# Kernel tuning notes

Hardware: AMD Instinct MI355X
Metric: run time of the kernel (lower is better)

## Reference

```python
import jax, jax.numpy as jnp
import numpy as np

B, S, T, V, E, H, D, A = 16, 128, 128, 32000, 512, 512, 512, 512
ENC = 2 * H  # bidirectional encoder output dim
NEG = -1e9


def _w(key, shape, scale=0.05):
    return scale * jax.random.normal(key, shape, dtype=jnp.float32)


def setup_inputs() -> dict:
    key = jax.random.key(0)
    ks = jax.random.split(key, 26)
    src = jax.random.randint(ks[0], (B, S), 1, V)
    tgt = jax.random.randint(ks[1], (B, T), 1, V)
    src_lens = jnp.full((B,), S, dtype=jnp.int32)  # full-length sequences (pack == identity)
    return dict(
        src=src, src_lens=src_lens, tgt=tgt,
        enc_embed=_w(ks[2], (V, E)).at[0].set(0.0),   # padding_idx=0
        Wih_f=_w(ks[3], (4 * H, E)), Whh_f=_w(ks[4], (4 * H, H)),
        bih_f=_w(ks[5], (4 * H,)), bhh_f=_w(ks[6], (4 * H,)),
        Wih_b=_w(ks[7], (4 * H, E)), Whh_b=_w(ks[8], (4 * H, H)),
        bih_b=_w(ks[9], (4 * H,)), bhh_b=_w(ks[10], (4 * H,)),
        Wbh=_w(ks[11], (D, 2 * H)), bbh=_w(ks[12], (D,)),
        Wbc=_w(ks[13], (D, 2 * H)), bbc=_w(ks[14], (D,)),
        Wh_att=_w(ks[15], (A, ENC)), Ws_att=_w(ks[16], (A, D)), v_att=_w(ks[17], (A,)),
        dec_embed=_w(ks[18], (V, E)).at[0].set(0.0),  # padding_idx=0
        Wih_d=_w(ks[19], (4 * D, E + ENC)), Whh_d=_w(ks[20], (4 * D, D)),
        bih_d=_w(ks[21], (4 * D,)), bhh_d=_w(ks[22], (4 * D,)),
        Wfc=_w(ks[23], (V, D + ENC)), bfc=_w(ks[24], (V,)),
    )


def _lstm_cell(x, h, c, Wih, Whh, bih, bhh):
    # PyTorch gate order: i, f, g, o
    g = x @ Wih.T + h @ Whh.T + (bih + bhh)
    i, f, gg, o = jnp.split(g, 4, axis=-1)
    c = jax.nn.sigmoid(f) * c + jax.nn.sigmoid(i) * jnp.tanh(gg)
    h = jax.nn.sigmoid(o) * jnp.tanh(c)
    return h, c


def _run_lstm(xs, Wih, Whh, bih, bhh, hdim):
    # xs: [S, B, E] -> (hs [S, B, hdim], h_last, c_last)
    b = xs.shape[1]
    h0 = jnp.zeros((b, hdim), xs.dtype)

    def step(carry, x):
        h, c = carry
        h, c = _lstm_cell(x, h, c, Wih, Whh, bih, bhh)
        return (h, c), h

    (hT, cT), hs = jax.lax.scan(step, (h0, h0), xs)
    return hs, hT, cT


def reference(src, src_lens, tgt, enc_embed, Wih_f, Whh_f, bih_f, bhh_f,
              Wih_b, Whh_b, bih_b, bhh_b, Wbh, bbh, Wbc, bbc,
              Wh_att, Ws_att, v_att, dec_embed, Wih_d, Whh_d, bih_d, bhh_d,
              Wfc, bfc):
    # ---- BiLSTM encoder (src_lens == S, so packing is the identity) ----
    emb = enc_embed[src]                      # [B, S, E]
    xs = jnp.swapaxes(emb, 0, 1)              # [S, B, E]
    hs_f, hf, _ = _run_lstm(xs, Wih_f, Whh_f, bih_f, bhh_f, H)
    hs_b, hb, _ = _run_lstm(xs[::-1], Wih_b, Whh_b, bih_b, bhh_b, H)
    hs_b = hs_b[::-1]
    enc_out = jnp.swapaxes(jnp.concatenate([hs_f, hs_b], axis=-1), 0, 1)  # [B, S, 2H]

    # ---- bridge (num_layers = 1) ----
    h_cat = jnp.concatenate([hf, hb], axis=-1)  # [B, 2H]
    h0 = jnp.tanh(h_cat @ Wbh.T + bbh)          # [B, D]
    c_cat = jnp.concatenate([hf, hb], axis=-1)
    c0 = jnp.tanh(c_cat @ Wbc.T + bbc)

    mask = jnp.arange(S)[None, :] < src_lens[:, None]  # [B, S]
    enc_proj = jnp.einsum('bse,ae->bsa', enc_out, Wh_att)  # W_h(enc_out), hoisted

    # ---- decoder loop, teacher_forcing = 1.0 ----
    def dec_step(carry, inp_t):
        h, c = carry
        # Bahdanau attention on top-layer hidden state
        score = jnp.einsum('bsa,a->bs', jnp.tanh(enc_proj + (h @ Ws_att.T)[:, None, :]), v_att)
        score = jnp.where(mask, score, NEG)
        attn = jax.nn.softmax(score, axis=-1)
        ctx = jnp.einsum('bs,bse->be', attn, enc_out)       # [B, 2H]
        x = jnp.concatenate([dec_embed[inp_t], ctx], axis=-1)  # [B, E+2H]
        h, c = _lstm_cell(x, h, c, Wih_d, Whh_d, bih_d, bhh_d)
        logits = jnp.concatenate([h, ctx], axis=-1) @ Wfc.T + bfc  # [B, V]
        return (h, c), logits

    inps = tgt[:, :-1].T  # [T-1, B]
    _, logits = jax.lax.scan(dec_step, (h0, c0), inps)
    return jnp.swapaxes(logits, 0, 1)  # [B, T-1, V]
```

## Files before the change

kernel.cpp:

```cpp
#include <hip/hip_runtime.h>

typedef __bf16 bf16x8 __attribute__((ext_vector_type(8)));
typedef float f32x4 __attribute__((ext_vector_type(4)));
typedef unsigned short us;
typedef unsigned long long ull;

#define DEV static __device__ __forceinline__

DEV float bf2f(us u){ union { unsigned u; float f; } x; x.u = ((unsigned)u) << 16; return x.f; }
DEV us f2bf(float f){
  union { float f; unsigned u; } x; x.f = f;
  unsigned r = x.u + 0x7fffu + ((x.u >> 16) & 1u);
  return (us)(r >> 16);
}
DEV unsigned pack2(us lo, us hi){ return (unsigned)lo | ((unsigned)hi << 16); }
DEV float sigm(float x){ return 1.0f / (1.0f + expf(-x)); }
DEV float tanh_fast(float x){ float e = __expf(2.0f * x); return 1.0f - 2.0f / (e + 1.0f); }
DEV void unpk2(unsigned u, float& a, float& b){ a = bf2f((us)u); b = bf2f((us)(u >> 16)); }

DEV unsigned ld4v(const unsigned* p){ return __hip_atomic_load(p, __ATOMIC_RELAXED, __HIP_MEMORY_SCOPE_AGENT); }
DEV ull ld8v(const void* p){ return __hip_atomic_load((const ull*)p, __ATOMIC_RELAXED, __HIP_MEMORY_SCOPE_AGENT); }
DEV void st4v(unsigned* p, unsigned v){ __hip_atomic_store(p, v, __ATOMIC_RELAXED, __HIP_MEMORY_SCOPE_AGENT); }

DEV void gridbar3(unsigned* arr, unsigned ep){
  __syncthreads();
  if (threadIdx.x == 0)
    __hip_atomic_store(arr + (size_t)blockIdx.x * 16, ep, __ATOMIC_RELEASE, __HIP_MEMORY_SCOPE_AGENT);
  if (threadIdx.x < 128){
    while (__hip_atomic_load(arr + (size_t)threadIdx.x * 16, __ATOMIC_RELAXED, __HIP_MEMORY_SCOPE_AGENT) < ep)
      __builtin_amdgcn_s_sleep(4);
  }
  __syncthreads();
}

DEV void groupbar(unsigned* gbase, int slot, unsigned ep){
  __syncthreads();
  if (threadIdx.x == 0)
    __hip_atomic_store(gbase + slot * 16, ep, __ATOMIC_RELEASE, __HIP_MEMORY_SCOPE_AGENT);
  if (threadIdx.x < 8){
    while (__hip_atomic_load(gbase + threadIdx.x * 16, __ATOMIC_RELAXED, __HIP_MEMORY_SCOPE_AGENT) < ep)
      __builtin_amdgcn_s_sleep(2);
  }
  __syncthreads();
}

__global__ void k_f2bf(const float4* __restrict__ in, uint2* __restrict__ out, long n4){
  long stride = (long)gridDim.x * blockDim.x;
  for (long i = (long)blockIdx.x * blockDim.x + threadIdx.x; i < n4; i += stride){
    float4 v = in[i];
    uint2 o; o.x = pack2(f2bf(v.x), f2bf(v.y)); o.y = pack2(f2bf(v.z), f2bf(v.w));
    out[i] = o;
  }
}

__global__ void k_bias3(const float* a0, const float* b0, float* o0,
                        const float* a1, const float* b1, float* o1,
                        const float* a2, const float* b2, float* o2){
  int i = blockIdx.x * 256 + threadIdx.x;
  o0[i] = a0[i] + b0[i];
  o1[i] = a1[i] + b1[i];
  o2[i] = a2[i] + b2[i];
}

__global__ void k_embed(const int* __restrict__ tok, const float* __restrict__ table,
                        us* __restrict__ out){
  int r = blockIdx.x;
  int b = r & 15, pos = r >> 4;
  int idx = tok[b * 128 + pos];
  float4 v = ((const float4*)(table + (size_t)idx * 512))[threadIdx.x];
  uint2 o; o.x = pack2(f2bf(v.x), f2bf(v.y)); o.y = pack2(f2bf(v.z), f2bf(v.w));
  ((uint2*)(out + (size_t)r * 512))[threadIdx.x] = o;
}

template<int MODE>
__global__ __launch_bounds__(256)
void gemm_bt(const us* __restrict__ A, int lda,
             const us* __restrict__ B, int ldb,
             const float* __restrict__ bias,
             void* __restrict__ Cv, int ldc, int K, int mvalid)
{
  __shared__ __align__(16) us As[128 * 64];
  __shared__ __align__(16) us Bs[128 * 64];
  const int tid  = threadIdx.x;
  const int lane = tid & 63, wid = tid >> 6;
  const int wm = (wid >> 1) * 64, wn = (wid & 1) * 64;
  const us* Ab = A + (size_t)blockIdx.y * 128 * lda;
  const us* Bb = B + (size_t)blockIdx.x * 128 * ldb;

  f32x4 acc[4][4] = {};
  bf16x8 ga[4], gb[4];

  #pragma unroll
  for (int r = 0; r < 4; r++){
    int c = tid + r * 256;
    ga[r] = *(const bf16x8*)(Ab + (size_t)(c >> 3) * lda + (c & 7) * 8);
    gb[r] = *(const bf16x8*)(Bb + (size_t)(c >> 3) * ldb + (c & 7) * 8);
  }
  const int nt = K >> 6;
  for (int t = 0; t < nt; t++){
    #pragma unroll
    for (int r = 0; r < 4; r++){
      int c = tid + r * 256;
      int slot = ((c >> 3) * 8 + ((c & 7) ^ ((c >> 3) & 7))) * 8;
      *(bf16x8*)(As + slot) = ga[r];
      *(bf16x8*)(Bs + slot) = gb[r];
    }
    __syncthreads();
    if (t + 1 < nt){
      int k0 = (t + 1) * 64;
      #pragma unroll
      for (int r = 0; r < 4; r++){
        int c = tid + r * 256;
        ga[r] = *(const bf16x8*)(Ab + (size_t)(c >> 3) * lda + k0 + (c & 7) * 8);
        gb[r] = *(const bf16x8*)(Bb + (size_t)(c >> 3) * ldb + k0 + (c & 7) * 8);
      }
    }
    #pragma unroll
    for (int kk = 0; kk < 2; kk++){
      bf16x8 av[4], bv[4];
      #pragma unroll
      for (int i = 0; i < 4; i++){
        int ra = wm + i * 16 + (lane & 15);
        int ua = (kk * 4 + (lane >> 4)) ^ (ra & 7);
        av[i] = *(const bf16x8*)(As + (ra * 8 + ua) * 8);
        int rb = wn + i * 16 + (lane & 15);
        int ub = (kk * 4 + (lane >> 4)) ^ (rb & 7);
        bv[i] = *(const bf16x8*)(Bs + (rb * 8 + ub) * 8);
      }
      #pragma unroll
      for (int i = 0; i < 4; i++)
        #pragma unroll
        for (int j = 0; j < 4; j++)
          acc[i][j] = __builtin_amdgcn_mfma_f32_16x16x32_bf16(av[i], bv[j], acc[i][j], 0, 0, 0);
    }
    if (t + 1 < nt) __syncthreads();
  }

  const int cb = lane & 15, rb4 = (lane >> 4) * 4;
  #pragma unroll
  for (int i = 0; i < 4; i++){
    #pragma unroll
    for (int j = 0; j < 4; j++){
      #pragma unroll
      for (int r = 0; r < 4; r++){
        int row = blockIdx.y * 128 + wm + i * 16 + rb4 + r;
        int col = blockIdx.x * 128 + wn + j * 16 + cb;
        float v = acc[i][j][r];
        if (bias) v += bias[col];
        if (MODE == 0) ((float*)Cv)[(size_t)row * ldc + col] = v;
        else           ((us*)Cv)[(size_t)row * ldc + col] = f2bf(v);
      }
    }
  }
}

__global__ __launch_bounds__(256)
void enc_persist4(const float* __restrict__ gin_f, const float* __restrict__ gin_b,
                  const us* __restrict__ whhf_bf, const us* __restrict__ whhb_bf,
                  us* __restrict__ enc_out_bf,
                  unsigned* __restrict__ arr)
{
  __shared__ __align__(16) us Wt[2][1024][8];
  __shared__ __align__(16) us Hrow[2][16][520];
  __shared__ __align__(16) f32x4 P[2][4][64];
  __shared__ float gl[2][16][17];
  __shared__ float hvout[2][16][4];

  const int bx = blockIdx.x, tid = threadIdx.x;
  const int lane = tid & 63, wv = tid >> 6;

  for (int d = 0; d < 2; d++){
    const us* srcw = d ? whhb_bf : whhf_bf;
    for (int u = tid; u < 1024; u += 256){
      int ks = u >> 6, ch = (u >> 4) & 3, v = u & 15;
      int n = (v & 3) * 512 + bx * 4 + (v >> 2);
      *(bf16x8*)Wt[d][u] = *(const bf16x8*)(srcw + (size_t)n * 512 + ks * 32 + ch * 8);
    }
  }

  float creg = 0.0f;
  const int cd = (tid >> 6) & 1, cb = tid & 15, cj = (tid >> 4) & 3;

  for (int t = 0; t < 128; t++){
    if (t == 0){
      #pragma unroll
      for (int r = 0; r < 8; r++){
        int u = tid + r * 256;
        int d = u >> 10, b = (u >> 6) & 15, s16 = u & 63;
        *(ull*)&Hrow[d][b][s16 * 8]     = 0ull;
        *(ull*)&Hrow[d][b][s16 * 8 + 4] = 0ull;
      }
    } else {
      #pragma unroll
      for (int r = 0; r < 8; r++){
        int u = tid + r * 256;
        int d = u >> 10, b = (u >> 6) & 15, s16 = u & 63;
        int sp = d ? (128 - t) : (t - 1);
        const us* s = enc_out_bf + ((size_t)b * 128 + sp) * 1024 + d * 512 + s16 * 8;
        ull lo = ld8v(s), hi = ld8v(s + 4);
        *(ull*)&Hrow[d][b][s16 * 8]     = lo;
        *(ull*)&Hrow[d][b][s16 * 8 + 4] = hi;
      }
    }
    __syncthreads();
    #pragma unroll
    for (int d = 0; d < 2; d++){
      f32x4 acc = {};
      #pragma unroll
      for (int m = 0; m < 4; m++){
        int ks = wv * 4 + m;
        int ch = lane >> 4, b = lane & 15;
        acc = __builtin_amdgcn_mfma_f32_16x16x32_bf16(*(const bf16x8*)&Hrow[d][b][ks * 32 + ch * 8],
                                                      *(const bf16x8*)Wt[d][(ks * 4 + ch) * 16 + b],
                                                      acc, 0, 0, 0);
      }
      P[d][wv][lane] = acc;
    }
    __syncthreads();
    if (wv < 2){
      int d = wv;
      f32x4 sum = (P[d][0][lane] + P[d][1][lane]) + (P[d][2][lane] + P[d][3][lane]);
      int v = lane & 15;
      int n = (v & 3) * 512 + bx * 4 + (v >> 2);
      int s_in = d ? (127 - t) : t;
      const float* gg = (d ? gin_b : gin_f) + (size_t)s_in * 16 * 2048 + n;
      #pragma unroll
      for (int r = 0; r < 4; r++){
        int b = (lane >> 4) * 4 + r;
        gl[d][v][b] = sum[r] + gg[(size_t)b * 2048];
      }
    }
    __syncthreads();
    if (tid < 128){
      float ig = sigm (gl[cd][cj * 4 + 0][cb]);
      float fg = sigm (gl[cd][cj * 4 + 1][cb]);
      float g2 = tanhf(gl[cd][cj * 4 + 2][cb]);
      float og = sigm (gl[cd][cj * 4 + 3][cb]);
      float cn = fg * creg + ig * g2;
      float hv = og * tanhf(cn);
      creg = cn;
      hvout[cd][cb][cj] = hv;
    }
    __syncthreads();
    if (tid < 64){
      int d = tid >> 5, rem = tid & 31, b = rem & 15, jp = rem >> 4;
      int s_in = d ? (127 - t) : t;
      st4v((unsigned*)(enc_out_bf + ((size_t)b * 128 + s_in) * 1024 + d * 512 + bx * 4 + jp * 2),
           pack2(f2bf(hvout[d][b][jp * 2]), f2bf(hvout[d][b][jp * 2 + 1])));
    }
    if (t != 127) gridbar3(arr, t + 1);
  }
}

__global__ __launch_bounds__(512)
void k_h0c0(const us* __restrict__ enc_out_bf, const float* __restrict__ Wbh, const float* __restrict__ bbh,
            const float* __restrict__ Wbc, const float* __restrict__ bbc,
            us* __restrict__ h0_bf, float* __restrict__ c_dec)
{
  __shared__ float hc[1024];
  int b = blockIdx.x >> 1, which = blockIdx.x & 1;
  int tid = threadIdx.x;
  hc[tid]       = bf2f(enc_out_bf[((size_t)b * 128 + 127) * 1024 + tid]);
  hc[512 + tid] = bf2f(enc_out_bf[((size_t)b * 128 + 0)   * 1024 + 512 + tid]);
  __syncthreads();
  const float* W = which ? Wbc : Wbh;
  float acc = (which ? bbc : bbh)[tid];
  const float* wr = W + (size_t)tid * 1024;
  for (int k = 0; k < 1024; k += 4){
    float4 w = *(const float4*)(wr + k);
    acc += w.x * hc[k] + w.y * hc[k + 1] + w.z * hc[k + 2] + w.w * hc[k + 3];
  }
  float v = tanhf(acc);
  if (which) c_dec[b * 512 + tid] = v;
  else       h0_bf[b * 512 + tid] = f2bf(v);
}

#define SMEM_BYTES 162464

__global__ __launch_bounds__(256)
void dec_fused3(const us* __restrict__ h0_bf, const float* __restrict__ c_dec0,
                const float* __restrict__ Ws_att, const float* __restrict__ v_att,
                const us* __restrict__ enc_proj_bf, const us* __restrict__ enc_out_bf,
                const int* __restrict__ src_lens, const float* __restrict__ gin_d,
                const us* __restrict__ whhd_bf, const us* __restrict__ wihd_bf,
                float* __restrict__ pscore_g,
                us* __restrict__ hctx,
                const us* __restrict__ wfc, const float* __restrict__ bfc,
                float* __restrict__ out,
                unsigned* __restrict__ arr, unsigned* __restrict__ arrG,
                unsigned* __restrict__ tdone)
{
  __shared__ __align__(16) char smem[SMEM_BYTES];
  const int tid = threadIdx.x;

  if (blockIdx.x >= 128){
    us* As = (us*)smem;
    us* Bs = (us*)(smem + 32768);
    const int lane = tid & 63, wid = tid >> 6;
    const int wm = wid * 64;
    for (int tile = blockIdx.x - 128; tile < 2000; tile += 128){
      int rt = tile / 250, ct = tile - rt * 250;
      unsigned need = (rt == 7) ? 127u : (unsigned)(16 * rt + 16);
      if (tid == 0){
        while (ld4v(tdone) < need) __builtin_amdgcn_s_sleep(8);
      }
      __syncthreads();
      const us* Ab = hctx + (size_t)rt * 256 * 1536;
      const us* Bb = wfc  + (size_t)ct * 128 * 1536;
      f32x4 acc[4][8] = {};
      bf16x8 ga[8], gb[4];
      #pragma unroll
      for (int r = 0; r < 8; r++){
        int cc = tid + r * 256;
        int row = cc >> 3, piece = cc & 7;
        bool val = (rt * 256 + row) < 2032;
        union { ull q[2]; bf16x8 v; } u;
        const us* p = Ab + (size_t)row * 1536 + piece * 8;
        u.q[0] = val ? ld8v(p) : 0ull;
        u.q[1] = val ? ld8v(p + 4) : 0ull;
        ga[r] = u.v;
      }
      #pragma unroll
      for (int r = 0; r < 4; r++){
        int cc = tid + r * 256;
        gb[r] = __builtin_nontemporal_load((const bf16x8*)(Bb + (size_t)(cc >> 3) * 1536 + (cc & 7) * 8));
      }
      for (int tk = 0; tk < 24; tk++){
        #pragma unroll
        for (int r = 0; r < 8; r++){
          int cc = tid + r * 256;
          int slot = ((cc >> 3) * 8 + ((cc & 7) ^ ((cc >> 3) & 7))) * 8;
          *(bf16x8*)(As + slot) = ga[r];
        }
        #pragma unroll
        for (int r = 0; r < 4; r++){
          int cc = tid + r * 256;
          int slot = ((cc >> 3) * 8 + ((cc & 7) ^ ((cc >> 3) & 7))) * 8;
          *(bf16x8*)(Bs + slot) = gb[r];
        }
        __syncthreads();
        if (tk + 1 < 24){
          int k0 = (tk + 1) * 64;
          #pragma unroll
          for (int r = 0; r < 8; r++){
            int cc = tid + r * 256;
            int row = cc >> 3, piece = cc & 7;
            bool val = (rt * 256 + row) < 2032;
            union { ull q[2]; bf16x8 v; } u;
            const us* p = Ab + (size_t)row * 1536 + k0 + piece * 8;
            u.q[0] = val ? ld8v(p) : 0ull;
            u.q[1] = val ? ld8v(p + 4) : 0ull;
            ga[r] = u.v;
          }
          #pragma unroll
          for (int r = 0; r < 4; r++){
            int cc = tid + r * 256;
            gb[r] = __builtin_nontemporal_load((const bf16x8*)(Bb + (size_t)(cc >> 3) * 1536 + k0 + (cc & 7) * 8));
          }
        }
        #pragma unroll
        for (int kk = 0; kk < 2; kk++){
          bf16x8 av[4], bv[8];
          #pragma unroll
          for (int i = 0; i < 4; i++){
            int ra = wm + i * 16 + (lane & 15);
            int ua = (kk * 4 + (lane >> 4)) ^ (ra & 7);
            av[i] = *(const bf16x8*)(As + (ra * 8 + ua) * 8);
          }
          #pragma unroll
          for (int j = 0; j < 8; j++){
            int rb = j * 16 + (lane & 15);
            int ub = (kk * 4 + (lane >> 4)) ^ (rb & 7);
            bv[j] = *(const bf16x8*)(Bs + (rb * 8 + ub) * 8);
          }
          #pragma unroll
          for (int i = 0; i < 4; i++)
            #pragma unroll
            for (int j = 0; j < 8; j++)
              acc[i][j] = __builtin_amdgcn_mfma_f32_16x16x32_bf16(av[i], bv[j], acc[i][j], 0, 0, 0);
        }
        if (tk + 1 < 24) __syncthreads();
      }
      const int cbl = lane & 15, rb4 = (lane >> 4) * 4;
      #pragma unroll
      for (int i = 0; i < 4; i++){
        #pragma unroll
        for (int j = 0; j < 8; j++){
          #pragma unroll
          for (int r = 0; r < 4; r++){
            int row = rt * 256 + wm + i * 16 + rb4 + r;
            int col = ct * 128 + j * 16 + cbl;
            if (row < 2032){
              float v = acc[i][j][r] + bfc[col];
              int tt = row >> 4, b = row & 15;
              out[((size_t)b * 127 + tt) * 32000 + col] = v;
            }
          }
        }
      }
    }
    return;
  }

  us (*Wh)[8]      = (us(*)[8])(smem);
  us (*Wc)[8]      = (us(*)[8])(smem + 16384);
  us (*Ws64)[520]  = (us(*)[520])(smem + 49152);
  us (*Xrow)[1032] = (us(*)[1032])(smem + 115712);
  f32x4 (*P)[64]   = (f32x4(*)[64])(smem + 148736);
  float (*g1l)[17] = (float(*)[17])(smem + 152832);
  float (*gl)[17]  = (float(*)[17])(smem + 153920);
  float* vl64      = (float*)(smem + 155008);
  float (*hsp)[64] = (float(*)[64])(smem + 155264);
  float* hs_own    = (float*)(smem + 156288);
  float (*pall)[128] = (float(*)[128])(smem + 156544);
  float* att       = (float*)(smem + 160640);
  float (*cred)[128] = (float(*)[128])(smem + 161152);
  float* sred      = (float*)(smem + 162176);
  float (*hvs)[4]  = (float(*)[4])(smem + 162208);

  const int bx = blockIdx.x;
  const int lane = tid & 63, wv = tid >> 6;
  const int bB = bx & 15, sQ = bx >> 4;
  unsigned* gbase = arrG + bB * 128;

  for (int u = tid; u < 1024; u += 256){
    int ks = u >> 6, ch = (u >> 4) & 3, v = u & 15;
    int n = (v & 3) * 512 + bx * 4 + (v >> 2);
    *(bf16x8*)Wh[u] = *(const bf16x8*)(whhd_bf + (size_t)n * 512 + ks * 32 + ch * 8);
  }
  for (int u = tid; u < 2048; u += 256){
    int ks = u >> 6, ch = (u >> 4) & 3, v = u & 15;
    int n = (v & 3) * 512 + bx * 4 + (v >> 2);
    *(bf16x8*)Wc[u] = *(const bf16x8*)(wihd_bf + (size_t)n * 1536 + 512 + ks * 32 + ch * 8);
  }
  for (int u = tid; u < 32768; u += 256){
    int a = u >> 9, k = u & 511;
    Ws64[a][k] = f2bf(Ws_att[(size_t)(sQ * 64 + a) * 512 + k]);
  }
  if (tid < 64) vl64[tid] = v_att[sQ * 64 + tid];
  const int slen = src_lens[bB];

  float creg = 0.0f;
  if (tid < 64) creg = c_dec0[(tid & 15) * 512 + bx * 4 + (tid >> 4)];

  for (int t = 0; t < 127; t++){
    const us* hsrc = t ? (hctx + (size_t)(t - 1) * 16 * 1536) : h0_bf;
    const int hstride = t ? 1536 : 512;

    #pragma unroll
    for (int r = 0; r < 4; r++){
      int u = tid + r * 256;
      int b = u >> 6, s16 = u & 63;
      const us* s = hsrc + (size_t)b * hstride + s16 * 8;
      ull lo = ld8v(s), hi = ld8v(s + 4);
      *(ull*)&Xrow[b][s16 * 8]     = lo;
      *(ull*)&Xrow[b][s16 * 8 + 4] = hi;
    }
    __syncthreads();
    {
      f32x4 acc = {};
      #pragma unroll
      for (int m = 0; m < 4; m++){
        int ks = wv * 4 + m;
        int ch = lane >> 4, b = lane & 15;
        acc = __builtin_amdgcn_mfma_f32_16x16x32_bf16(*(const bf16x8*)&Xrow[b][ks * 32 + ch * 8],
                                                      *(const bf16x8*)Wh[(ks * 4 + ch) * 16 + b],
                                                      acc, 0, 0, 0);
      }
      P[wv][lane] = acc;
    }
    {
      const us* wr = Ws64[lane] + wv * 128;
      const us* xr = Xrow[bB] + wv * 128;
      float s = 0.f;
      #pragma unroll
      for (int k = 0; k < 128; k += 8){
        bf16x8 xv = *(const bf16x8*)(xr + k);
        bf16x8 wv8 = *(const bf16x8*)(wr + k);
        #pragma unroll
        for (int e = 0; e < 8; e++) s += (float)xv[e] * (float)wv8[e];
      }
      hsp[wv][lane] = s;
    }
    __syncthreads();
    if (wv == 0){
      f32x4 sum = (P[0][lane] + P[1][lane]) + (P[2][lane] + P[3][lane]);
      int v = lane & 15;
      int n = (v & 3) * 512 + bx * 4 + (v >> 2);
      #pragma unroll
      for (int r = 0; r < 4; r++){
        int b = (lane >> 4) * 4 + r;
        g1l[v][b] = sum[r] + gin_d[((size_t)t * 16 + b) * 2048 + n];
      }
    }
    if (tid < 64) hs_own[tid] = hsp[0][tid] + hsp[1][tid] + hsp[2][tid] + hsp[3][tid];
    __syncthreads();
    {
      int s = tid >> 1, half = tid & 1;
      const us* er = enc_proj_bf + ((size_t)bB * 128 + s) * 512 + sQ * 64 + half * 32;
      const float* hb = hs_own + half * 32;
      const float* vp = vl64 + half * 32;
      float sv = 0.f;
      #pragma unroll
      for (int a = 0; a < 32; a += 8){
        uint4 u4 = *(const uint4*)(er + a);
        float e0,e1,e2,e3,e4,e5,e6,e7;
        unpk2(u4.x,e0,e1); unpk2(u4.y,e2,e3); unpk2(u4.z,e4,e5); unpk2(u4.w,e6,e7);
        sv += vp[a+0]*tanh_fast(e0+hb[a+0]) + vp[a+1]*tanh_fast(e1+hb[a+1])
            + vp[a+2]*tanh_fast(e2+hb[a+2]) + vp[a+3]*tanh_fast(e3+hb[a+3])
            + vp[a+4]*tanh_fast(e4+hb[a+4]) + vp[a+5]*tanh_fast(e5+hb[a+5])
            + vp[a+6]*tanh_fast(e6+hb[a+6]) + vp[a+7]*tanh_fast(e7+hb[a+7]);
      }
      sv += __shfl_xor(sv, 1);
      if (half == 0)
        st4v((unsigned*)&pscore_g[(size_t)bB * 1024 + sQ * 128 + s], __float_as_uint(sv));
    }

    groupbar(gbase, sQ, t + 1);

    for (int u = tid; u < 1024; u += 256)
      (&pall[0][0])[u] = __uint_as_float(ld4v((unsigned*)&pscore_g[(size_t)bB * 1024 + u]));
    __syncthreads();
    {
      float e = 0.f;
      if (tid < 128){
        float sc = ((pall[0][tid] + pall[1][tid]) + (pall[2][tid] + pall[3][tid]))
                 + ((pall[4][tid] + pall[5][tid]) + (pall[6][tid] + pall[7][tid]));
        e = (tid < slen) ? __expf(sc) : 0.f;
        att[tid] = e;
      }
      float ss = e;
      #pragma unroll
      for (int o = 32; o; o >>= 1) ss += __shfl_xor(ss, o);
      if (lane == 0) sred[wv] = ss;
    }
    __syncthreads();
    {
      int kk = tid & 127, half = tid >> 7;
      const float* ab = att + half * 64;
      const us* er = enc_out_bf + ((size_t)(bB * 128 + half * 64)) * 1024 + sQ * 128 + kk;
      float s = 0.f;
      #pragma unroll 8
      for (int s2 = 0; s2 < 64; s2++)
        s += ab[s2] * bf2f(er[(size_t)s2 * 1024]);
      cred[half][kk] = s;
    }
    __syncthreads();
    if (tid < 64){
      float inv = 1.0f / (sred[0] + sred[1] + sred[2] + sred[3]);
      int kk2 = tid * 2;
      float c0 = (cred[0][kk2]     + cred[1][kk2])     * inv;
      float c1 = (cred[0][kk2 + 1] + cred[1][kk2 + 1]) * inv;
      st4v((unsigned*)(hctx + ((size_t)t * 16 + bB) * 1536 + 512 + sQ * 128 + kk2),
           pack2(f2bf(c0), f2bf(c1)));
    }

    gridbar3(arr, 2 * t + 1);

    #pragma unroll
    for (int r = 0; r < 8; r++){
      int u = tid + r * 256;
      int b = u >> 7, s16 = u & 127;
      const us* s = hctx + ((size_t)t * 16 + b) * 1536 + 512 + s16 * 8;
      ull lo = ld8v(s), hi = ld8v(s + 4);
      *(ull*)&Xrow[b][s16 * 8]     = lo;
      *(ull*)&Xrow[b][s16 * 8 + 4] = hi;
    }
    __syncthreads();
    {
      f32x4 acc = {};
      #pragma unroll
      for (int m = 0; m < 8; m++){
        int ks = wv * 8 + m;
        int ch = lane >> 4, b = lane & 15;
        acc = __builtin_amdgcn_mfma_f32_16x16x32_bf16(*(const bf16x8*)&Xrow[b][ks * 32 + ch * 8],
                                                      *(const bf16x8*)Wc[(ks * 4 + ch) * 16 + b],
                                                      acc, 0, 0, 0);
      }
      P[wv][lane] = acc;
    }
    __syncthreads();
    if (wv == 0){
      f32x4 sum = (P[0][lane] + P[1][lane]) + (P[2][lane] + P[3][lane]);
      int v = lane & 15;
      #pragma unroll
      for (int r = 0; r < 4; r++){
        int b = (lane >> 4) * 4 + r;
        gl[v][b] = sum[r] + g1l[v][b];
      }
    }
    __syncthreads();
    if (tid < 64){
      int b2 = tid & 15, joff = tid >> 4;
      float ig = sigm (gl[joff * 4 + 0][b2]);
      float fg = sigm (gl[joff * 4 + 1][b2]);
      float g2 = tanhf(gl[joff * 4 + 2][b2]);
      float og = sigm (gl[joff * 4 + 3][b2]);
      float cn = fg * creg + ig * g2;
      float hv = og * tanhf(cn);
      creg = cn;
      hvs[b2][joff] = hv;
    }
    __syncthreads();
    if (tid < 32){
      int b = tid & 15, jp = tid >> 4;
      st4v((unsigned*)(hctx + ((size_t)t * 16 + b) * 1536 + bx * 4 + jp * 2),
           pack2(f2bf(hvs[b][jp * 2]), f2bf(hvs[b][jp * 2 + 1])));
    }
    gridbar3(arr, 2 * t + 2);
    if (bx == 0 && tid == 0)
      __hip_atomic_store(tdone, (unsigned)(t + 1), __ATOMIC_RELEASE, __HIP_MEMORY_SCOPE_AGENT);
  }
}

extern "C" void kernel_launch(void* const* d_in, const int* in_sizes, int n_in,
                              void* d_out, int out_size, void* d_ws, size_t ws_size,
                              hipStream_t stream)
{
  const int*   src       = (const int*)d_in[0];
  const int*   src_lens  = (const int*)d_in[1];
  const int*   tgt       = (const int*)d_in[2];
  const float* enc_embed = (const float*)d_in[3];
  const float* Wih_f = (const float*)d_in[4];
  const float* Whh_f = (const float*)d_in[5];
  const float* bih_f = (const float*)d_in[6];
  const float* bhh_f = (const float*)d_in[7];
  const float* Wih_b = (const float*)d_in[8];
  const float* Whh_b = (const float*)d_in[9];
  const float* bih_b = (const float*)d_in[10];
  const float* bhh_b = (const float*)d_in[11];
  const float* Wbh = (const float*)d_in[12];
  const float* bbh = (const float*)d_in[13];
  const float* Wbc = (const float*)d_in[14];
  const float* bbc = (const float*)d_in[15];
  const float* Wh_att = (const float*)d_in[16];
  const float* Ws_att = (const float*)d_in[17];
  const float* v_att  = (const float*)d_in[18];
  const float* dec_embed = (const float*)d_in[19];
  const float* Wih_d = (const float*)d_in[20];
  const float* Whh_d = (const float*)d_in[21];
  const float* bih_d = (const float*)d_in[22];
  const float* bhh_d = (const float*)d_in[23];
  const float* Wfc = (const float*)d_in[24];
  const float* bfc = (const float*)d_in[25];
  float* out = (float*)d_out;

  char* base = (char*)d_ws;
  size_t off = 0;
  auto take = [&](size_t bytes) -> char* {
    char* p = base + off;
    off += (bytes + 255) & ~(size_t)255;
    return p;
  };
  us* wfc_bf    = (us*)take((size_t)32000 * 1536 * 2);
  us* emb_e     = (us*)take((size_t)2048 * 512 * 2);
  us* emb_d     = (us*)take((size_t)2048 * 512 * 2);
  us* wihf_bf   = (us*)take((size_t)2048 * 512 * 2);
  us* wihb_bf   = (us*)take((size_t)2048 * 512 * 2);
  us* wihd_bf   = (us*)take((size_t)2048 * 1536 * 2);
  us* whhf_bf   = (us*)take((size_t)2048 * 512 * 2);
  us* whhb_bf   = (us*)take((size_t)2048 * 512 * 2);
  us* whhd_bf   = (us*)take((size_t)2048 * 512 * 2);
  us* whatt_bf  = (us*)take((size_t)512 * 1024 * 2);
  float* gin_f    = (float*)take((size_t)2048 * 2048 * 4);
  float* gin_b    = (float*)take((size_t)2048 * 2048 * 4);
  float* gin_d    = (float*)take((size_t)2048 * 2048 * 4);
  us* enc_out_bf  = (us*)take((size_t)2048 * 1024 * 2);
  us* enc_proj_bf = (us*)take((size_t)2048 * 512 * 2);
  us* hctx        = (us*)take((size_t)2048 * 1536 * 2);
  us* h0_bf       = (us*)take((size_t)16 * 512 * 2);
  float* c_dec    = (float*)take((size_t)16 * 512 * 4);
  float* pscore_g = (float*)take((size_t)16 * 1024 * 4);
  float* bias_f = (float*)take(2048 * 4);
  float* bias_b = (float*)take(2048 * 4);
  float* bias_d = (float*)take(2048 * 4);
  unsigned* arrE  = (unsigned*)take(128 * 16 * 4);
  unsigned* arrD  = (unsigned*)take(128 * 16 * 4);
  unsigned* arrG  = (unsigned*)take(16 * 8 * 16 * 4);
  unsigned* tdone = (unsigned*)take(256);

  hipMemsetAsync(emb_d, 0, (size_t)2048 * 512 * 2, stream);
  hipMemsetAsync(hctx, 0, (size_t)2048 * 1536 * 2, stream);
  hipMemsetAsync(arrE, 0, (128 * 16 + 128 * 16 + 16 * 8 * 16) * 4 + 256, stream);

  k_f2bf<<<4096, 256, 0, stream>>>((const float4*)Wfc,   (uint2*)wfc_bf,   (long)32000 * 1536 / 4);
  k_f2bf<<<512,  256, 0, stream>>>((const float4*)Wih_f, (uint2*)wihf_bf,  (long)2048 * 512 / 4);
  k_f2bf<<<512,  256, 0, stream>>>((const float4*)Wih_b, (uint2*)wihb_bf,  (long)2048 * 512 / 4);
  k_f2bf<<<1024, 256, 0, stream>>>((const float4*)Wih_d, (uint2*)wihd_bf,  (long)2048 * 1536 / 4);
  k_f2bf<<<512,  256, 0, stream>>>((const float4*)Whh_f, (uint2*)whhf_bf,  (long)2048 * 512 / 4);
  k_f2bf<<<512,  256, 0, stream>>>((const float4*)Whh_b, (uint2*)whhb_bf,  (long)2048 * 512 / 4);
  k_f2bf<<<512,  256, 0, stream>>>((const float4*)Whh_d, (uint2*)whhd_bf,  (long)2048 * 512 / 4);
  k_f2bf<<<512,  256, 0, stream>>>((const float4*)Wh_att,(uint2*)whatt_bf, (long)512 * 1024 / 4);
  k_bias3<<<8, 256, 0, stream>>>(bih_f, bhh_f, bias_f, bih_b, bhh_b, bias_b, bih_d, bhh_d, bias_d);

  k_embed<<<2048, 128, 0, stream>>>(src, enc_embed, emb_e);
  k_embed<<<2032, 128, 0, stream>>>(tgt, dec_embed, emb_d);

  gemm_bt<0><<<dim3(16, 16), 256, 0, stream>>>(emb_e, 512, wihf_bf, 512,  bias_f, gin_f, 2048, 512, 4096);
  gemm_bt<0><<<dim3(16, 16), 256, 0, stream>>>(emb_e, 512, wihb_bf, 512,  bias_b, gin_b, 2048, 512, 4096);
  gemm_bt<0><<<dim3(16, 16), 256, 0, stream>>>(emb_d, 512, wihd_bf, 1536, bias_d, gin_d, 2048, 512, 4096);

  enc_persist4<<<128, 256, 0, stream>>>(gin_f, gin_b, whhf_bf, whhb_bf, enc_out_bf, arrE);

  k_h0c0<<<32, 512, 0, stream>>>(enc_out_bf, Wbh, bbh, Wbc, bbc, h0_bf, c_dec);

  gemm_bt<2><<<dim3(4, 16), 256, 0, stream>>>(enc_out_bf, 1024, whatt_bf, 1024, nullptr, enc_proj_bf, 512, 1024, 4096);

  dec_fused3<<<256, 256, 0, stream>>>(h0_bf, c_dec, Ws_att, v_att, enc_proj_bf, enc_out_bf, src_lens,
                                      gin_d, whhd_bf, wihd_bf, pscore_g, hctx,
                                      wfc_bf, bfc, out, arrD, arrG, tdone);
}
```

Before: 3.678 ms.

## Split encoder barrier per direction, overlap decoder group barrier with Whh MFMA

The encoder persistent kernel now gives each block one direction with 8 hidden units, so the forward and backward LSTMs synchronise on separate 64-block barriers instead of one 128-block grid barrier. In the decoder, the group barrier is split into signal and wait halves, and the recurrent MFMA plus the gate partial sums are moved between them to hide barrier latency. The context reduction is rewritten to use vectorized bf16x8 loads with a 16-way shared-memory reduction, and the partial-score gather uses 8-byte loads. Each encoder block now loads only one direction's hidden row, but the wider tile per block and the extra shared-memory staging could shift timing.

Result: faster. 3.166 ms (-13.9%).

```diff
diff --git a/kernel.cpp b/kernel.cpp
--- a/kernel.cpp
+++ b/kernel.cpp
@@ -22,24 +22,40 @@
 DEV ull ld8v(const void* p){ return __hip_atomic_load((const ull*)p, __ATOMIC_RELAXED, __HIP_MEMORY_SCOPE_AGENT); }
 DEV void st4v(unsigned* p, unsigned v){ __hip_atomic_store(p, v, __ATOMIC_RELAXED, __HIP_MEMORY_SCOPE_AGENT); }
 
-DEV void gridbar3(unsigned* arr, unsigned ep){
+DEV void barS(unsigned* arr, unsigned ep){
   __syncthreads();
   if (threadIdx.x == 0)
     __hip_atomic_store(arr + (size_t)blockIdx.x * 16, ep, __ATOMIC_RELEASE, __HIP_MEMORY_SCOPE_AGENT);
+}
+DEV void barW(unsigned* arr, unsigned ep){
   if (threadIdx.x < 128){
     while (__hip_atomic_load(arr + (size_t)threadIdx.x * 16, __ATOMIC_RELAXED, __HIP_MEMORY_SCOPE_AGENT) < ep)
       __builtin_amdgcn_s_sleep(4);
   }
   __syncthreads();
 }
-
-DEV void groupbar(unsigned* gbase, int slot, unsigned ep){
+DEV void gridbar3(unsigned* arr, unsigned ep){ barS(arr, ep); barW(arr, ep); }
+
+DEV void gbarS(unsigned* gbase, int slot, unsigned ep){
   __syncthreads();
   if (threadIdx.x == 0)
     __hip_atomic_store(gbase + slot * 16, ep, __ATOMIC_RELEASE, __HIP_MEMORY_SCOPE_AGENT);
+}
+DEV void gbarW(unsigned* gbase, unsigned ep){
   if (threadIdx.x < 8){
     while (__hip_atomic_load(gbase + threadIdx.x * 16, __ATOMIC_RELAXED, __HIP_MEMORY_SCOPE_AGENT) < ep)
       __builtin_amdgcn_s_sleep(2);
+  }
+  __syncthreads();
+}
+
+DEV void encbar64(unsigned* arr, int bl, unsigned ep){
+  __syncthreads();
+  if (threadIdx.x == 0)
+    __hip_atomic_store(arr + (size_t)bl * 16, ep, __ATOMIC_RELEASE, __HIP_MEMORY_SCOPE_AGENT);
+  if (threadIdx.x < 64){
+    while (__hip_atomic_load(arr + (size_t)threadIdx.x * 16, __ATOMIC_RELAXED, __HIP_MEMORY_SCOPE_AGENT) < ep)
+      __builtin_amdgcn_s_sleep(4);
   }
   __syncthreads();
 }
@@ -155,100 +171,103 @@
 }
 
 __global__ __launch_bounds__(256)
-void enc_persist4(const float* __restrict__ gin_f, const float* __restrict__ gin_b,
+void enc_persist5(const float* __restrict__ gin_f, const float* __restrict__ gin_b,
                   const us* __restrict__ whhf_bf, const us* __restrict__ whhb_bf,
                   us* __restrict__ enc_out_bf,
-                  unsigned* __restrict__ arr)
+                  unsigned* __restrict__ arrF, unsigned* __restrict__ arrB)
 {
   __shared__ __align__(16) us Wt[2][1024][8];
-  __shared__ __align__(16) us Hrow[2][16][520];
+  __shared__ __align__(16) us Hrow[16][520];
   __shared__ __align__(16) f32x4 P[2][4][64];
   __shared__ float gl[2][16][17];
-  __shared__ float hvout[2][16][4];
+  __shared__ float hvout[16][8];
 
   const int bx = blockIdx.x, tid = threadIdx.x;
   const int lane = tid & 63, wv = tid >> 6;
-
-  for (int d = 0; d < 2; d++){
-    const us* srcw = d ? whhb_bf : whhf_bf;
+  const int dir = bx >> 6, bl = bx & 63;
+  unsigned* arr = dir ? arrB : arrF;
+  const us* whh = dir ? whhb_bf : whhf_bf;
+  const float* gin = dir ? gin_b : gin_f;
+
+  for (int ti = 0; ti < 2; ti++)
     for (int u = tid; u < 1024; u += 256){
       int ks = u >> 6, ch = (u >> 4) & 3, v = u & 15;
-      int n = (v & 3) * 512 + bx * 4 + (v >> 2);
-      *(bf16x8*)Wt[d][u] = *(const bf16x8*)(srcw + (size_t)n * 512 + ks * 32 + ch * 8);
-    }
-  }
+      int n = (v & 3) * 512 + bl * 8 + ti * 4 + (v >> 2);
+      *(bf16x8*)Wt[ti][u] = *(const bf16x8*)(whh + (size_t)n * 512 + ks * 32 + ch * 8);
+    }
 
   float creg = 0.0f;
-  const int cd = (tid >> 6) & 1, cb = tid & 15, cj = (tid >> 4) & 3;
+  const int cb = tid & 15, cjo = (tid >> 4) & 7;
 
   for (int t = 0; t < 128; t++){
     if (t == 0){
       #pragma unroll
-      for (int r = 0; r < 8; r++){
+      for (int r = 0; r < 4; r++){
         int u = tid + r * 256;
-        int d = u >> 10, b = (u >> 6) & 15, s16 = u & 63;
-        *(ull*)&Hrow[d][b][s16 * 8]     = 0ull;
-        *(ull*)&Hrow[d][b][s16 * 8 + 4] = 0ull;
+        int b = u >> 6, s16 = u & 63;
+        *(ull*)&Hrow[b][s16 * 8]     = 0ull;
+        *(ull*)&Hrow[b][s16 * 8 + 4] = 0ull;
       }
     } else {
-      #pragma unroll
-      for (int r = 0; r < 8; r++){
+      int sp = dir ? (128 - t) : (t - 1);
+      #pragma unroll
+      for (int r = 0; r < 4; r++){
         int u = tid + r * 256;
-        int d = u >> 10, b = (u >> 6) & 15, s16 = u & 63;
-        int sp = d ? (128 - t) : (t - 1);
-        const us* s = enc_out_bf + ((size_t)b * 128 + sp) * 1024 + d * 512 + s16 * 8;
+        int b = u >> 6, s16 = u & 63;
+        const us* s = enc_out_bf + ((size_t)b * 128 + sp) * 1024 + dir * 512 + s16 * 8;
         ull lo = ld8v(s), hi = ld8v(s + 4);
-        *(ull*)&Hrow[d][b][s16 * 8]     = lo;
-        *(ull*)&Hrow[d][b][s16 * 8 + 4] = hi;
+        *(ull*)&Hrow[b][s16 * 8]     = lo;
+        *(ull*)&Hrow[b][s16 * 8 + 4] = hi;
       }
     }
     __syncthreads();
     #pragma unroll
-    for (int d = 0; d < 2; d++){
+    for (int ti = 0; ti < 2; ti++){
       f32x4 acc = {};
       #pragma unroll
       for (int m = 0; m < 4; m++){
         int ks = wv * 4 + m;
         int ch = lane >> 4, b = lane & 15;
-        acc = __builtin_amdgcn_mfma_f32_16x16x32_bf16(*(const bf16x8*)&Hrow[d][b][ks * 32 + ch * 8],
-                                                      *(const bf16x8*)Wt[d][(ks * 4 + ch) * 16 + b],
+        acc = __builtin_amdgcn_mfma_f32_16x16x32_bf16(*(const bf16x8*)&Hrow[b][ks * 32 + ch * 8],
+                                                      *(const bf16x8*)Wt[ti][(ks * 4 + ch) * 16 + b],
                                                       acc, 0, 0, 0);
       }
-      P[d][wv][lane] = acc;
+      P[ti][wv][lane] = acc;
     }
     __syncthreads();
     if (wv < 2){
-      int d = wv;
-      f32x4 sum = (P[d][0][lane] + P[d][1][lane]) + (P[d][2][lane] + P[d][3][lane]);
+      int ti = wv;
+      f32x4 sum = (P[ti][0][lane] + P[ti][1][lane]) + (P[ti][2][lane] + P[ti][3][lane]);
       int v = lane & 15;
-      int n = (v & 3) * 512 + bx * 4 + (v >> 2);
-      int s_in = d ? (127 - t) : t;
-      const float* gg = (d ? gin_b : gin_f) + (size_t)s_in * 16 * 2048 + n;
+      int n = (v & 3) * 512 + bl * 8 + ti * 4 + (v >> 2);
+      int s_in = dir ? (127 - t) : t;
+      const float* gg = gin + (size_t)s_in * 16 * 2048 + n;
       #pragma unroll
       for (int r = 0; r < 4; r++){
         int b = (lane >> 4) * 4 + r;
-        gl[d][v][b] = sum[r] + gg[(size_t)b * 2048];
+        gl[ti][v][b] = sum[r] + gg[(size_t)b * 2048];
       }
     }
     __syncthreads();
     if (tid < 128){
-      float ig = sigm (gl[cd][cj * 4 + 0][cb]);
-      float fg = sigm (gl[cd][cj * 4 + 1][cb]);
-      float g2 = tanhf(gl[cd][cj * 4 + 2][cb]);
-      float og = sigm (gl[cd][cj * 4 + 3][cb]);
+      int ti = cjo >> 2, jr = cjo & 3;
+      float ig = sigm (gl[ti][jr * 4 + 0][cb]);
+      float fg = sigm (gl[ti][jr * 4 + 1][cb]);
+      float g2 = tanhf(gl[ti][jr * 4 + 2][cb]);
+      float og = sigm (gl[ti][jr * 4 + 3][cb]);
       float cn = fg * creg + ig * g2;
       float hv = og * tanhf(cn);
       creg = cn;
-      hvout[cd][cb][cj] = hv;
+      hvout[cb][cjo] = hv;
     }
     __syncthreads();
     if (tid < 64){
-      int d = tid >> 5, rem = tid & 31, b = rem & 15, jp = rem >> 4;
-      int s_in = d ? (127 - t) : t;
-      st4v((unsigned*)(enc_out_bf + ((size_t)b * 128 + s_in) * 1024 + d * 512 + bx * 4 + jp * 2),
-           pack2(f2bf(hvout[d][b][jp * 2]), f2bf(hvout[d][b][jp * 2 + 1])));
-    }
-    if (t != 127) gridbar3(arr, t + 1);
+      int b = tid & 15, jp = tid >> 4;
+      int s_in = dir ? (127 - t) : t;
+      st4v((unsigned*)(enc_out_bf + ((size_t)b * 128 + s_in) * 1024 + dir * 512 + bl * 8 + jp * 2),
+           pack2(f2bf(hvout[b][jp * 2]), f2bf(hvout[b][jp * 2 + 1])));
+    }
+    if (t != 127) encbar64(arr, bl, t + 1);
   }
 }
 
@@ -275,10 +294,10 @@
   else       h0_bf[b * 512 + tid] = f2bf(v);
 }
 
-#define SMEM_BYTES 162464
+#define SMEM_BYTES 161440
 
 __global__ __launch_bounds__(256)
-void dec_fused3(const us* __restrict__ h0_bf, const float* __restrict__ c_dec0,
+void dec_fused5(const us* __restrict__ h0_bf, const float* __restrict__ c_dec0,
                 const float* __restrict__ Ws_att, const float* __restrict__ v_att,
                 const us* __restrict__ enc_proj_bf, const us* __restrict__ enc_out_bf,
                 const int* __restrict__ src_lens, const float* __restrict__ gin_d,
@@ -406,6 +425,7 @@
   us (*Wc)[8]      = (us(*)[8])(smem + 16384);
   us (*Ws64)[520]  = (us(*)[520])(smem + 49152);
   us (*Xrow)[1032] = (us(*)[1032])(smem + 115712);
+  float (*credv)[132] = (float(*)[132])(smem + 115712);
   f32x4 (*P)[64]   = (f32x4(*)[64])(smem + 148736);
   float (*g1l)[17] = (float(*)[17])(smem + 152832);
   float (*gl)[17]  = (float(*)[17])(smem + 153920);
@@ -413,10 +433,9 @@
   float (*hsp)[64] = (float(*)[64])(smem + 155264);
   float* hs_own    = (float*)(smem + 156288);
   float (*pall)[128] = (float(*)[128])(smem + 156544);
-  float* att       = (float*)(smem + 160640);
-  float (*cred)[128] = (float(*)[128])(smem + 161152);
-  float* sred      = (float*)(smem + 162176);
-  float (*hvs)[4]  = (float(*)[4])(smem + 162208);
+  float* e_own     = (float*)(smem + 160640);
+  float* sred      = (float*)(smem + 161152);
+  float (*hvs)[4]  = (float(*)[4])(smem + 161184);
 
   const int bx = blockIdx.x;
   const int lane = tid & 63, wv = tid >> 6;
@@ -458,18 +477,6 @@
     }
     __syncthreads();
     {
-      f32x4 acc = {};
-      #pragma unroll
-      for (int m = 0; m < 4; m++){
-        int ks = wv * 4 + m;
-        int ch = lane >> 4, b = lane & 15;
-        acc = __builtin_amdgcn_mfma_f32_16x16x32_bf16(*(const bf16x8*)&Xrow[b][ks * 32 + ch * 8],
-                                                      *(const bf16x8*)Wh[(ks * 4 + ch) * 16 + b],
-                                                      acc, 0, 0, 0);
-      }
-      P[wv][lane] = acc;
-    }
-    {
       const us* wr = Ws64[lane] + wv * 128;
       const us* xr = Xrow[bB] + wv * 128;
       float s = 0.f;
@@ -483,16 +490,6 @@
       hsp[wv][lane] = s;
     }
     __syncthreads();
-    if (wv == 0){
-      f32x4 sum = (P[0][lane] + P[1][lane]) + (P[2][lane] + P[3][lane]);
-      int v = lane & 15;
-      int n = (v & 3) * 512 + bx * 4 + (v >> 2);
-      #pragma unroll
-      for (int r = 0; r < 4; r++){
-        int b = (lane >> 4) * 4 + r;
-        g1l[v][b] = sum[r] + gin_d[((size_t)t * 16 + b) * 2048 + n];
-      }
-    }
     if (tid < 64) hs_own[tid] = hsp[0][tid] + hsp[1][tid] + hsp[2][tid] + hsp[3][tid];
     __syncthreads();
     {
@@ -515,11 +512,35 @@
       if (half == 0)
         st4v((unsigned*)&pscore_g[(size_t)bB * 1024 + sQ * 128 + s], __float_as_uint(sv));
     }
-
-    groupbar(gbase, sQ, t + 1);
-
-    for (int u = tid; u < 1024; u += 256)
-      (&pall[0][0])[u] = __uint_as_float(ld4v((unsigned*)&pscore_g[(size_t)bB * 1024 + u]));
+    gbarS(gbase, sQ, t + 1);
+
+    {
+      f32x4 acc = {};
+      #pragma unroll
+      for (int m = 0; m < 4; m++){
+        int ks = wv * 4 + m;
+        int ch = lane >> 4, b = lane & 15;
+        acc = __builtin_amdgcn_mfma_f32_16x16x32_bf16(*(const bf16x8*)&Xrow[b][ks * 32 + ch * 8],
+                                                      *(const bf16x8*)Wh[(ks * 4 + ch) * 16 + b],
+                                                      acc, 0, 0, 0);
+      }
+      P[wv][lane] = acc;
+    }
+    __syncthreads();
+    if (wv == 0){
+      f32x4 sum = (P[0][lane] + P[1][lane]) + (P[2][lane] + P[3][lane]);
+      int v = lane & 15;
+      int n = (v & 3) * 512 + bx * 4 + (v >> 2);
+      #pragma unroll
+      for (int r = 0; r < 4; r++){
+        int b = (lane >> 4) * 4 + r;
+        g1l[v][b] = sum[r] + gin_d[((size_t)t * 16 + b) * 2048 + n];
+      }
+    }
+    gbarW(gbase, t + 1);
+
+    for (int u = tid; u < 512; u += 256)
+      ((ull*)&pall[0][0])[u] = ld8v(&pscore_g[(size_t)bB * 1024 + u * 2]);
     __syncthreads();
     {
       float e = 0.f;
@@ -527,7 +548,7 @@
         float sc = ((pall[0][tid] + pall[1][tid]) + (pall[2][tid] + pall[3][tid]))
                  + ((pall[4][tid] + pall[5][tid]) + (pall[6][tid] + pall[7][tid]));
         e = (tid < slen) ? __expf(sc) : 0.f;
-        att[tid] = e;
+        e_own[tid] = e;
       }
       float ss = e;
       #pragma unroll
@@ -536,25 +557,35 @@
     }
     __syncthreads();
     {
-      int kk = tid & 127, half = tid >> 7;
-      const float* ab = att + half * 64;
-      const us* er = enc_out_bf + ((size_t)(bB * 128 + half * 64)) * 1024 + sQ * 128 + kk;
-      float s = 0.f;
-      #pragma unroll 8
-      for (int s2 = 0; s2 < 64; s2++)
-        s += ab[s2] * bf2f(er[(size_t)s2 * 1024]);
-      cred[half][kk] = s;
+      int sg = tid >> 4, kb = tid & 15;
+      const us* base = enc_out_bf + ((size_t)(bB * 128 + sg * 8)) * 1024 + sQ * 128 + kb * 8;
+      f32x4 a0 = {}, a1 = {};
+      #pragma unroll
+      for (int si = 0; si < 8; si++){
+        bf16x8 v = *(const bf16x8*)(base + (size_t)si * 1024);
+        float ev = e_own[sg * 8 + si];
+        a0[0] += ev * (float)v[0]; a0[1] += ev * (float)v[1];
+        a0[2] += ev * (float)v[2]; a0[3] += ev * (float)v[3];
+        a1[0] += ev * (float)v[4]; a1[1] += ev * (float)v[5];
+        a1[2] += ev * (float)v[6]; a1[3] += ev * (float)v[7];
+      }
+      *(f32x4*)&credv[sg][kb * 8]     = a0;
+      *(f32x4*)&credv[sg][kb * 8 + 4] = a1;
     }
     __syncthreads();
     if (tid < 64){
-      float inv = 1.0f / (sred[0] + sred[1] + sred[2] + sred[3]);
-      int kk2 = tid * 2;
-      float c0 = (cred[0][kk2]     + cred[1][kk2])     * inv;
-      float c1 = (cred[0][kk2 + 1] + cred[1][kk2 + 1]) * inv;
-      st4v((unsigned*)(hctx + ((size_t)t * 16 + bB) * 1536 + 512 + sQ * 128 + kk2),
+      float inv = 1.0f / ((sred[0] + sred[1]) + (sred[2] + sred[3]));
+      int k2 = tid * 2;
+      float c0 = 0.f, c1 = 0.f;
+      #pragma unroll
+      for (int r = 0; r < 16; r++){
+        float2 p = *(const float2*)&credv[r][k2];
+        c0 += p.x; c1 += p.y;
+      }
+      c0 *= inv; c1 *= inv;
+      st4v((unsigned*)(hctx + ((size_t)t * 16 + bB) * 1536 + 512 + sQ * 128 + k2),
            pack2(f2bf(c0), f2bf(c1)));
     }
-
     gridbar3(arr, 2 * t + 1);
 
     #pragma unroll
@@ -674,14 +705,15 @@
   float* bias_f = (float*)take(2048 * 4);
   float* bias_b = (float*)take(2048 * 4);
   float* bias_d = (float*)take(2048 * 4);
-  unsigned* arrE  = (unsigned*)take(128 * 16 * 4);
+  unsigned* arrF  = (unsigned*)take(64 * 16 * 4);
+  unsigned* arrB  = (unsigned*)take(64 * 16 * 4);
   unsigned* arrD  = (unsigned*)take(128 * 16 * 4);
   unsigned* arrG  = (unsigned*)take(16 * 8 * 16 * 4);
   unsigned* tdone = (unsigned*)take(256);
 
   hipMemsetAsync(emb_d, 0, (size_t)2048 * 512 * 2, stream);
   hipMemsetAsync(hctx, 0, (size_t)2048 * 1536 * 2, stream);
-  hipMemsetAsync(arrE, 0, (128 * 16 + 128 * 16 + 16 * 8 * 16) * 4 + 256, stream);
+  hipMemsetAsync(arrF, 0, (64 * 16 + 64 * 16 + 128 * 16 + 16 * 8 * 16) * 4 + 256, stream);
 
   k_f2bf<<<4096, 256, 0, stream>>>((const float4*)Wfc,   (uint2*)wfc_bf,   (long)32000 * 1536 / 4);
   k_f2bf<<<512,  256, 0, stream>>>((const float4*)Wih_f, (uint2*)wihf_bf,  (long)2048 * 512 / 4);
@@ -700,13 +732,13 @@
   gemm_bt<0><<<dim3(16, 16), 256, 0, stream>>>(emb_e, 512, wihb_bf, 512,  bias_b, gin_b, 2048, 512, 4096);
   gemm_bt<0><<<dim3(16, 16), 256, 0, stream>>>(emb_d, 512, wihd_bf, 1536, bias_d, gin_d, 2048, 512, 4096);
 
-  enc_persist4<<<128, 256, 0, stream>>>(gin_f, gin_b, whhf_bf, whhb_bf, enc_out_bf, arrE);
+  enc_persist5<<<128, 256, 0, stream>>>(gin_f, gin_b, whhf_bf, whhb_bf, enc_out_bf, arrF, arrB);
 
   k_h0c0<<<32, 512, 0, stream>>>(enc_out_bf, Wbh, bbh, Wbc, bbc, h0_bf, c_dec);
 
   gemm_bt<2><<<dim3(4, 16), 256, 0, stream>>>(enc_out_bf, 1024, whatt_bf, 1024, nullptr, enc_proj_bf, 512, 1024, 4096);
 
-  dec_fused3<<<256, 256, 0, stream>>>(h0_bf, c_dec, Ws_att, v_att, enc_proj_bf, enc_out_bf, src_lens,
+  dec_fused5<<<256, 256, 0, stream>>>(h0_bf, c_dec, Ws_att, v_att, enc_proj_bf, enc_out_bf, src_lens,
                                       gin_d, whhd_bf, wihd_bf, pscore_g, hctx,
                                       wfc_bf, bfc, out, arrD, arrG, tdone);
 }
```
